# Kernel optimization log

Measured on AMD Instinct MI355X. Metric: run time of the kernel, lower is better.

## Reference

```python
import jax, jax.numpy as jnp
import numpy as np

TEMPERATURE = 0.07
MARGIN = 0.2
EPS = 1e-8  # matches torch F.cosine_similarity eps


def _cosine_matrix(a, b):
    # a: (N, D), b: (M, D) -> (N, M) pairwise cosine similarity
    an = a / jnp.clip(jnp.linalg.norm(a, axis=-1, keepdims=True), EPS)
    bn = b / jnp.clip(jnp.linalg.norm(b, axis=-1, keepdims=True), EPS)
    return an @ bn.T


def setup_inputs() -> dict:
    key = jax.random.key(0)
    k1, k2, k3 = jax.random.split(key, 3)
    return {
        "step_embeddings": jax.random.normal(k1, (8192, 1024), dtype=jnp.float32),
        "modal_embeddings": jax.random.normal(k2, (4096, 1024), dtype=jnp.float32),
        "negative_modal_embeddings": jax.random.normal(k3, (4096, 1024), dtype=jnp.float32),
    }


def reference(step_embeddings, modal_embeddings, negative_modal_embeddings):
    # --- step-modal alignment (max cosine sim per step, averaged) ---
    S = _cosine_matrix(step_embeddings, modal_embeddings)        # (N, M)
    per_step = S.max(axis=1)                                      # (N,)
    alignment = per_step.mean()

    # --- attention-weighted alignment (use_attention=True) ---
    logits = (step_embeddings @ modal_embeddings.T) / TEMPERATURE  # (N, M)
    attention = jax.nn.softmax(logits, axis=1)
    weighted_alignment = (S * attention).sum(axis=1).mean()

    # --- contrastive coherence against negatives ---
    Sn = _cosine_matrix(step_embeddings, negative_modal_embeddings)
    negative_alignment = Sn.max(axis=1).mean()
    positive_alignment = alignment
    contrastive_score = positive_alignment - negative_alignment
    margin_score = jax.nn.relu(contrastive_score - MARGIN)

    # --- per-step coherence (same max-cosine per step) ---
    min_step_coherence = per_step.min()

    # overall uses weighted_alignment (attention on), mixed with contrastive
    overall = 0.7 * weighted_alignment + 0.3 * contrastive_score

    return (alignment, weighted_alignment, attention, contrastive_score,
            margin_score, positive_alignment, negative_alignment,
            per_step, min_step_coherence, overall)
```

## Files before the change

### kernel.cpp

```cpp
#include <hip/hip_runtime.h>
#include <cmath>


#define WAVE 64

typedef __bf16 bf16x8_t __attribute__((ext_vector_type(8)));
typedef __bf16 bf16x4_t __attribute__((ext_vector_type(4)));
typedef float f32x4_t __attribute__((ext_vector_type(4)));

__device__ __forceinline__ float wave_reduce_sum(float v) {
#pragma unroll
    for (int o = 32; o > 0; o >>= 1) v += __shfl_down(v, o, WAVE);
    return v;
}
__device__ __forceinline__ float wave_reduce_max(float v) {
#pragma unroll
    for (int o = 32; o > 0; o >>= 1) v = fmaxf(v, __shfl_down(v, o, WAVE));
    return v;
}
__device__ __forceinline__ float wave_reduce_min(float v) {
#pragma unroll
    for (int o = 32; o > 0; o >>= 1) v = fminf(v, __shfl_down(v, o, WAVE));
    return v;
}

__device__ __forceinline__ unsigned enc_f(float f) {
    unsigned u = __float_as_uint(f);
    return (u & 0x80000000u) ? ~u : (u | 0x80000000u);
}
__device__ __forceinline__ float dec_f(unsigned e) {
    unsigned u = (e & 0x80000000u) ? (e & 0x7fffffffu) : ~e;
    return __uint_as_float(u);
}

__global__ __launch_bounds__(256)
void convert_norms_kernel(const float* __restrict__ step,
                          const float* __restrict__ modal,
                          const float* __restrict__ negs,
                          char* __restrict__ arena,
                          float* __restrict__ ina, float* __restrict__ inb,
                          float* __restrict__ inn,
                          unsigned* __restrict__ negmax_u, int N, int M) {
    const int tid = threadIdx.x, lane = tid & 63, wv = tid >> 6;
    const int b = blockIdx.x * 4 + wv;
    const float* src;
    if (b < N)          src = step  + (size_t)b * 1024;
    else if (b < N + M) src = modal + (size_t)(b - N) * 1024;
    else                src = negs  + (size_t)(b - N - M) * 1024;

    char* cb = arena + (((size_t)(b >> 2)) << 14) + ((size_t)(b & 3) << 11) + 8192;
    float s = 0.0f;
#pragma unroll
    for (int q = 0; q < 4; q++) {
        const int idx = lane + q * 64;
        const float4 v = ((const float4*)src)[idx];
        bf16x4_t o;
        o[0] = (__bf16)v.x; o[1] = (__bf16)v.y;
        o[2] = (__bf16)v.z; o[3] = (__bf16)v.w;
        *(bf16x4_t*)(cb + (size_t)idx * 8) = o;
        s += v.x * v.x + v.y * v.y + v.z * v.z + v.w * v.w;
    }
    s = wave_reduce_sum(s);
    if (lane == 0) {
        const float inv = 1.0f / fmaxf(sqrtf(s), 1e-8f);
        if (b < N)          { ina[b] = inv; negmax_u[b] = 0u; }
        else if (b < N + M) inb[b - N] = inv;
        else                inn[b - N - M] = inv;
    }
}

#define GLD16(g, l)                                                       \
    __builtin_amdgcn_global_load_lds(                                     \
        (const __attribute__((address_space(1))) void*)(g),               \
        (__attribute__((address_space(3))) void*)(l), 16, 0, 0)

#define PIPE_BARRIER() asm volatile(                                      \
    "s_waitcnt vmcnt(0) lgkmcnt(0)\n\ts_barrier" ::: "memory")

__global__ __launch_bounds__(256, 2)
void gemm_fused_kernel(char* __restrict__ arena, int N, int M,
                       const float* __restrict__ inv_nn,
                       unsigned* __restrict__ negmax_u) {
    __shared__ __bf16 As[2][128 * 64];
    __shared__ __bf16 Bs[2][128 * 64];

    const int lin = blockIdx.x;
    const int nbn = (2 * M) >> 7;
    const int SBM = 32, SBN = 8, PER = SBM * SBN;
    const int sid = lin / PER;
    const int q   = lin % PER;
    const int bmi = q % SBM;
    const int bni = q / SBM;
    const int stn_per = nbn / SBN;
    const int bmg = sid / stn_per;
    const int stn = sid % stn_per;
    const int bm = (bmg * SBM + bmi) << 7;
    const int bn = (stn * SBN + bni) << 7;

    const int t = threadIdx.x, w = t >> 6, lane = t & 63;
    const int lane16 = lane & 15, lq = lane >> 4;
    const int wm = (w & 1) * 64, wn = (w >> 1) * 64;

    const int s_is_b  = w >> 1;
    const int rowbase = (w & 1) * 64;
    const int ln3 = lane >> 3;
    const int q_g = (lane & 7) ^ ln3;
    const int cbase = (s_is_b ? (N + bn) : bm) + rowbase;
    const int cc = cbase + ln3;
    const size_t off0 = (((size_t)(cc >> 2)) << 14) +
                        ((size_t)(cc & 3) << 11) + 8192 + (size_t)q_g * 16;
    const char* gbase = arena + off0;
    const int ldsoff = rowbase * 64;
    __bf16* ldsw0 = (s_is_b ? Bs[0] : As[0]) + ldsoff;
    __bf16* ldsw1 = (s_is_b ? Bs[1] : As[1]) + ldsoff;

    f32x4_t acc[4][4];
#pragma unroll
    for (int i = 0; i < 4; i++)
#pragma unroll
        for (int j = 0; j < 4; j++) acc[i][j] = (f32x4_t){0.f, 0.f, 0.f, 0.f};

    const int sxr = lane16 & 7;

#pragma unroll
    for (int r = 0; r < 8; r++)
        GLD16(gbase + (size_t)r * 32768, ldsw0 + r * 512);

    for (int it = 0; it < 16; ++it) {
        PIPE_BARRIER();
        const int cur = it & 1;

        if (it + 1 < 16) {
            const size_t k0b = (size_t)(it + 1) * 128;
            __bf16* ldsw = cur ? ldsw0 : ldsw1;
#pragma unroll
            for (int r = 0; r < 8; r++)
                GLD16(gbase + (size_t)r * 32768 + k0b, ldsw + r * 512);
        }

        bf16x8_t af[2][4], bf[2][4];
#pragma unroll
        for (int kk = 0; kk < 2; kk++) {
            const int qo = ((lq + kk * 4) ^ sxr) * 8;
#pragma unroll
            for (int i = 0; i < 4; i++)
                af[kk][i] = *(const bf16x8_t*)&As[cur][(wm + i * 16 + lane16) * 64 + qo];
#pragma unroll
            for (int j = 0; j < 4; j++)
                bf[kk][j] = *(const bf16x8_t*)&Bs[cur][(wn + j * 16 + lane16) * 64 + qo];
        }

#pragma unroll
        for (int kk = 0; kk < 2; kk++)
#pragma unroll
            for (int i = 0; i < 4; i++)
#pragma unroll
                for (int j = 0; j < 4; j++)
                    acc[i][j] = __builtin_amdgcn_mfma_f32_16x16x32_bf16(
                        af[kk][i], bf[kk][j], acc[i][j], 0, 0, 0);
    }

    if (bn < M) {
#pragma unroll
        for (int i = 0; i < 4; i++) {
#pragma unroll
            for (int r = 0; r < 4; r++) {
                const int grow = bm + wm + i * 16 + lq * 4 + r;
                __bf16* dst = (__bf16*)(arena + ((size_t)grow << 14)) +
                              bn + wn + lane16;
#pragma unroll
                for (int j = 0; j < 4; j++)
                    dst[j * 16] = (__bf16)acc[i][j][r];
            }
        }
    } else {
        float invn[4];
#pragma unroll
        for (int j = 0; j < 4; j++)
            invn[j] = inv_nn[(bn - M) + wn + j * 16 + lane16];
#pragma unroll
        for (int i = 0; i < 4; i++) {
#pragma unroll
            for (int r = 0; r < 4; r++) {
                float v = acc[i][0][r] * invn[0];
                v = fmaxf(v, acc[i][1][r] * invn[1]);
                v = fmaxf(v, acc[i][2][r] * invn[2]);
                v = fmaxf(v, acc[i][3][r] * invn[3]);
#pragma unroll
                for (int o = 8; o > 0; o >>= 1)
                    v = fmaxf(v, __shfl_xor(v, o, WAVE));
                if (lane16 == 0)
                    atomicMax(&negmax_u[bm + wm + i * 16 + lq * 4 + r], enc_f(v));
            }
        }
    }
}

#define CUT 2.0f
#define MAXCAND 64

__global__ __launch_bounds__(256)
void softmax_fix_kernel(char* __restrict__ arena, const float* __restrict__ step,
                        const float* __restrict__ modal,
                        const float* __restrict__ ina, const float* __restrict__ inb,
                        float* __restrict__ perstep, float* __restrict__ wout,
                        float* __restrict__ attn) {
    const int row = blockIdx.x, tid = threadIdx.x;
    const int lane = tid & 63, wv = tid >> 6;

    __shared__ float srow_s[1024];
    __shared__ float red[8];
    __shared__ float bcast[2];
    __shared__ int   cand[MAXCAND];
    __shared__ float exact[MAXCAND];
    __shared__ int   cnt;

    if (tid == 0) cnt = 0;
    ((float4*)srow_s)[tid] = ((const float4*)(step + (size_t)row * 1024))[tid];

    const __bf16* gb = (const __bf16*)(arena + ((size_t)row << 14));
    float vals[16];
    float invn[16];
#pragma unroll
    for (int g = 0; g < 4; g++) {
        const bf16x4_t v = *(const bf16x4_t*)(gb + g * 1024 + tid * 4);
        const float4 x = *(const float4*)(inb + g * 1024 + tid * 4);
        vals[g * 4 + 0] = (float)v[0]; vals[g * 4 + 1] = (float)v[1];
        vals[g * 4 + 2] = (float)v[2]; vals[g * 4 + 3] = (float)v[3];
        invn[g * 4 + 0] = x.x; invn[g * 4 + 1] = x.y;
        invn[g * 4 + 2] = x.z; invn[g * 4 + 3] = x.w;
    }

    float dmax = -3.4e38f;
#pragma unroll
    for (int j = 0; j < 16; j++) dmax = fmaxf(dmax, vals[j]);
    float wm = wave_reduce_max(dmax);
    if (lane == 0) red[wv] = wm;
    __syncthreads();
    if (tid == 0) bcast[0] = fmaxf(fmaxf(red[0], red[1]), fmaxf(red[2], red[3]));
    __syncthreads();
    const float m0 = bcast[0];

    const float thr = m0 - CUT;
#pragma unroll
    for (int g = 0; g < 4; g++)
#pragma unroll
        for (int u = 0; u < 4; u++) {
            if (vals[g * 4 + u] >= thr) {
                const int pos = atomicAdd(&cnt, 1);
                if (pos < MAXCAND) cand[pos] = g * 1024 + tid * 4 + u;
            }
        }
    __syncthreads();
    const int nc = min(cnt, MAXCAND);

    for (int i = wv; i < nc; i += 4) {
        const float* mrow = modal + (size_t)cand[i] * 1024;
        float p = 0.0f;
#pragma unroll
        for (int q = 0; q < 16; q++) {
            const int idx = lane + q * 64;
            p = fmaf(srow_s[idx], mrow[idx], p);
        }
        p = wave_reduce_sum(p);
        if (lane == 0) exact[i] = p;
    }
    __syncthreads();

    for (int i = 0; i < nc; i++) {
        const int c = cand[i];
        if (((c & 1023) >> 2) == tid) vals[(c >> 10) * 4 + (c & 3)] = exact[i];
    }

    float dmax2 = -3.4e38f, cmax = -3.4e38f;
#pragma unroll
    for (int j = 0; j < 16; j++) {
        dmax2 = fmaxf(dmax2, vals[j]);
        cmax = fmaxf(cmax, vals[j] * invn[j]);
    }
    float wg = wave_reduce_max(dmax2);
    float wc = wave_reduce_max(cmax);
    if (lane == 0) { red[wv] = wg; red[4 + wv] = wc; }
    __syncthreads();
    if (tid == 0) {
        bcast[0] = fmaxf(fmaxf(red[0], red[1]), fmaxf(red[2], red[3]));
        bcast[1] = fmaxf(fmaxf(red[4], red[5]), fmaxf(red[6], red[7]));
    }
    __syncthreads();
    const float invT = 1.0f / 0.07f;
    const float mlog = bcast[0] * invT;
    const float cmaxAll = bcast[1];

    float evals[16];
    float lsum = 0.0f;
#pragma unroll
    for (int j = 0; j < 16; j++) {
        const float e = __expf(vals[j] * invT - mlog);
        evals[j] = e;
        lsum += e;
    }
    lsum = wave_reduce_sum(lsum);
    __syncthreads();
    if (lane == 0) red[wv] = lsum;
    __syncthreads();
    if (tid == 0) bcast[0] = red[0] + red[1] + red[2] + red[3];
    __syncthreads();
    const float invZ = 1.0f / bcast[0];

    float* arow = attn + (size_t)row * 4096;
    float wacc = 0.0f;
#pragma unroll
    for (int g = 0; g < 4; g++) {
        float4 o;
        const float a0 = evals[g * 4 + 0] * invZ, a1 = evals[g * 4 + 1] * invZ;
        const float a2 = evals[g * 4 + 2] * invZ, a3 = evals[g * 4 + 3] * invZ;
        o.x = a0; o.y = a1; o.z = a2; o.w = a3;
        *(float4*)(arow + g * 1024 + tid * 4) = o;
        wacc += a0 * vals[g * 4 + 0] * invn[g * 4 + 0];
        wacc += a1 * vals[g * 4 + 1] * invn[g * 4 + 1];
        wacc += a2 * vals[g * 4 + 2] * invn[g * 4 + 2];
        wacc += a3 * vals[g * 4 + 3] * invn[g * 4 + 3];
    }
    wacc = wave_reduce_sum(wacc);
    __syncthreads();
    if (lane == 0) red[wv] = wacc;
    __syncthreads();
    if (tid == 0) {
        const float inv_na = ina[row];
        perstep[row] = cmaxAll * inv_na;
        wout[row] = (red[0] + red[1] + red[2] + red[3]) * inv_na;
    }
}

__global__ __launch_bounds__(1024)
void finalize_kernel(const float* __restrict__ perstep, const float* __restrict__ w,
                     const unsigned* __restrict__ negmax_u,
                     const float* __restrict__ ina, float* __restrict__ out,
                     int N, size_t NM) {
    float s_a = 0.0f, s_w = 0.0f, s_n = 0.0f, mn = 3.4e38f;
    for (int i = threadIdx.x; i < N; i += 1024) {
        const float p = perstep[i];
        s_a += p;
        s_w += w[i];
        s_n += dec_f(negmax_u[i]) * ina[i];
        mn = fminf(mn, p);
    }
    s_a = wave_reduce_sum(s_a);
    s_w = wave_reduce_sum(s_w);
    s_n = wave_reduce_sum(s_n);
    mn  = wave_reduce_min(mn);
    __shared__ float ra[16], rw[16], rn[16], rm[16];
    const int lane = threadIdx.x & 63, wv = threadIdx.x >> 6;
    if (lane == 0) { ra[wv] = s_a; rw[wv] = s_w; rn[wv] = s_n; rm[wv] = mn; }
    __syncthreads();
    if (threadIdx.x == 0) {
        float ta = 0, tw = 0, tn = 0, tm = 3.4e38f;
#pragma unroll
        for (int i = 0; i < 16; i++) {
            ta += ra[i]; tw += rw[i]; tn += rn[i]; tm = fminf(tm, rm[i]);
        }
        const float inv = 1.0f / (float)N;
        const float alignment = ta * inv;
        const float weighted  = tw * inv;
        const float neg       = tn * inv;
        const float contrast  = alignment - neg;
        const float margin    = fmaxf(contrast - 0.2f, 0.0f);
        const float overall   = 0.7f * weighted + 0.3f * contrast;
        out[0] = alignment;
        out[1] = weighted;
        float* p = out + 2 + NM;
        p[0] = contrast;
        p[1] = margin;
        p[2] = alignment;
        p[3] = neg;
        p[4 + N] = tm;
        p[5 + N] = overall;
    }
}

extern "C" void kernel_launch(void* const* d_in, const int* in_sizes, int n_in,
                              void* d_out, int out_size, void* d_ws, size_t ws_size,
                              hipStream_t stream) {
    const float* step  = (const float*)d_in[0];
    const float* modal = (const float*)d_in[1];
    const float* negs  = (const float*)d_in[2];
    float* out = (float*)d_out;

    const int K = 1024;
    const int N = in_sizes[0] / K;
    const int M = in_sizes[1] / K;
    const size_t NM = (size_t)N * (size_t)M;

    float* ina        = (float*)d_ws;
    float* inb        = ina + N;
    float* inn        = inb + M;
    unsigned* negmax  = (unsigned*)(inn + M);
    float* wsum       = (float*)(negmax + N);

    char* arena    = (char*)d_out + 16;
    float* attn    = out + 2;
    float* perstep = out + 2 + NM + 4;

    convert_norms_kernel<<<(N + 2 * M) / 4, 256, 0, stream>>>(
        step, modal, negs, arena, ina, inb, inn, negmax, N, M);

    const int nblocks = (N / 128) * ((2 * M) / 128);
    gemm_fused_kernel<<<nblocks, 256, 0, stream>>>(arena, N, M, inn, negmax);

    softmax_fix_kernel<<<N, 256, 0, stream>>>(arena, step, modal, ina, inb,
                                              perstep, wsum, attn);

    finalize_kernel<<<1, 1024, 0, stream>>>(perstep, wsum, negmax, ina, out, N, NM);
}
```

Baseline: 381.0 us.

## Enlarge GEMM tile to 256x256 with 8-wave ping-pong MFMA/load interleaving

```diff
diff --git a/kernel.cpp b/kernel.cpp
--- a/kernel.cpp
+++ b/kernel.cpp
@@ -74,100 +74,152 @@
         (const __attribute__((address_space(1))) void*)(g),               \
         (__attribute__((address_space(3))) void*)(l), 16, 0, 0)
 
-#define PIPE_BARRIER() asm volatile(                                      \
-    "s_waitcnt vmcnt(0) lgkmcnt(0)\n\ts_barrier" ::: "memory")
-
-__global__ __launch_bounds__(256, 2)
+#define BAR()   asm volatile("s_barrier" ::: "memory")
+#define LGKM0() asm volatile("s_waitcnt lgkmcnt(0)" ::: "memory")
+#define VMW(n)  asm volatile("s_waitcnt vmcnt(" #n ")" ::: "memory")
+
+#define STAGE_A(Ab, kt)                                                   \
+    _Pragma("unroll")                                                     \
+    for (int h = 0; h < 2; h++)                                           \
+    _Pragma("unroll")                                                     \
+      for (int c = 0; c < 2; c++)                                         \
+        GLD16(arena + srcA[h][c] + (size_t)(kt) * 128,                    \
+              (Ab) + h * 8192 + c * 4096 + w * 512);
+
+#define STAGE_B(Bb, kt)                                                   \
+    _Pragma("unroll")                                                     \
+    for (int h = 0; h < 2; h++)                                           \
+    _Pragma("unroll")                                                     \
+      for (int c = 0; c < 2; c++)                                         \
+        GLD16(arena + srcB[h][c] + (size_t)(kt) * 128,                    \
+              (Bb) + h * 8192 + c * 4096 + w * 512);
+
+#define READ_A(g, Ab)                                                     \
+    _Pragma("unroll")                                                     \
+    for (int ii = 0; ii < 4; ii++)                                        \
+    _Pragma("unroll")                                                     \
+      for (int kk = 0; kk < 2; kk++)                                      \
+        af[ii][kk] = *(const bf16x8_t*)&(Ab)[arow0 + (g) * 4096 +         \
+                                             ii * 1024 + koff[kk]];
+
+#define READ_B(j0, dst, Bb)                                               \
+    _Pragma("unroll")                                                     \
+    for (int jj = 0; jj < 2; jj++)                                        \
+    _Pragma("unroll")                                                     \
+      for (int kk = 0; kk < 2; kk++)                                      \
+        dst[jj][kk] = *(const bf16x8_t*)&(Bb)[brow0 + ((j0) + jj) * 1024 +\
+                                              koff[kk]];
+
+#define MFMA_Q(i0, j0, bsrc)                                              \
+    __builtin_amdgcn_s_setprio(1);                                        \
+    _Pragma("unroll")                                                     \
+    for (int kk = 0; kk < 2; kk++)                                        \
+    _Pragma("unroll")                                                     \
+      for (int ii = 0; ii < 4; ii++)                                      \
+      _Pragma("unroll")                                                   \
+        for (int jj = 0; jj < 2; jj++)                                    \
+          acc[(i0) + ii][(j0) + jj] =                                     \
+              __builtin_amdgcn_mfma_f32_16x16x32_bf16(                    \
+                  af[ii][kk], bsrc[jj][kk], acc[(i0) + ii][(j0) + jj],    \
+                  0, 0, 0);                                               \
+    __builtin_amdgcn_s_setprio(0);
+
+#define TILE(Ab, Bb, ktpre, pre)                                          \
+                                                             \
+    READ_A(0, Ab);                                                        \
+    READ_B(0, bf01, Bb);                                                  \
+    BAR(); LGKM0();                                                       \
+    MFMA_Q(0, 0, bf01);                                                   \
+    BAR();                                                                \
+                                                             \
+    READ_B(2, bf23, Bb);                                                  \
+    BAR(); LGKM0();                                                       \
+    MFMA_Q(0, 2, bf23);                                                   \
+    BAR();                                                                \
+     \
+    READ_A(1, Ab);                                                        \
+    if (pre) { STAGE_B(Bb, ktpre); }                                      \
+    BAR(); LGKM0();                                                       \
+    MFMA_Q(4, 0, bf01);                                                   \
+    BAR();                                                                \
+     \
+    if (pre) { STAGE_A(Ab, ktpre); }                                      \
+    BAR();                                                                \
+    MFMA_Q(4, 2, bf23);                                                   \
+    if (pre) { VMW(8); } else { VMW(0); }                                 \
+    BAR();
+
+__global__ __launch_bounds__(512, 2)
 void gemm_fused_kernel(char* __restrict__ arena, int N, int M,
                        const float* __restrict__ inv_nn,
                        unsigned* __restrict__ negmax_u) {
-    __shared__ __bf16 As[2][128 * 64];
-    __shared__ __bf16 Bs[2][128 * 64];
+    __shared__ __bf16 As[2][256 * 64];
+    __shared__ __bf16 Bs[2][256 * 64];
 
     const int lin = blockIdx.x;
-    const int nbn = (2 * M) >> 7;
-    const int SBM = 32, SBN = 8, PER = SBM * SBN;
-    const int sid = lin / PER;
-    const int q   = lin % PER;
-    const int bmi = q % SBM;
-    const int bni = q / SBM;
-    const int stn_per = nbn / SBN;
-    const int bmg = sid / stn_per;
-    const int stn = sid % stn_per;
-    const int bm = (bmg * SBM + bmi) << 7;
-    const int bn = (stn * SBN + bni) << 7;
+    const int sid = lin >> 5, qq = lin & 31;
+    const int bmi = qq & 7, bni = qq >> 3;
+    const int bmg = sid >> 3, stn = sid & 7;
+    const int bm = (bmg * 8 + bmi) << 8;
+    const int bn = (stn * 4 + bni) << 8;
 
     const int t = threadIdx.x, w = t >> 6, lane = t & 63;
     const int lane16 = lane & 15, lq = lane >> 4;
-    const int wm = (w & 1) * 64, wn = (w >> 1) * 64;
-
-    const int s_is_b  = w >> 1;
-    const int rowbase = (w & 1) * 64;
-    const int ln3 = lane >> 3;
-    const int q_g = (lane & 7) ^ ln3;
-    const int cbase = (s_is_b ? (N + bn) : bm) + rowbase;
-    const int cc = cbase + ln3;
-    const size_t off0 = (((size_t)(cc >> 2)) << 14) +
-                        ((size_t)(cc & 3) << 11) + 8192 + (size_t)q_g * 16;
-    const char* gbase = arena + off0;
-    const int ldsoff = rowbase * 64;
-    __bf16* ldsw0 = (s_is_b ? Bs[0] : As[0]) + ldsoff;
-    __bf16* ldsw1 = (s_is_b ? Bs[1] : As[1]) + ldsoff;
-
-    f32x4_t acc[4][4];
-#pragma unroll
-    for (int i = 0; i < 4; i++)
-#pragma unroll
-        for (int j = 0; j < 4; j++) acc[i][j] = (f32x4_t){0.f, 0.f, 0.f, 0.f};
+    const int wm = w >> 2, wn = w & 3;
+
+    const int l3 = lane >> 3, ol = lane & 7;
+    const int og = ol ^ l3;
+    unsigned srcA[2][2], srcB[2][2];
+#pragma unroll
+    for (int h = 0; h < 2; h++)
+#pragma unroll
+      for (int c = 0; c < 2; c++) {
+        const int ga = bm + h * 128 + c * 64 + w * 8 + l3;
+        srcA[h][c] = ((unsigned)(ga >> 2) << 14) + ((unsigned)(ga & 3) << 11)
+                     + 8192u + (unsigned)og * 16u;
+        const int gb = N + bn + h * 128 + c * 64 + w * 8 + l3;
+        srcB[h][c] = ((unsigned)(gb >> 2) << 14) + ((unsigned)(gb & 3) << 11)
+                     + 8192u + (unsigned)og * 16u;
+      }
 
     const int sxr = lane16 & 7;
-
-#pragma unroll
-    for (int r = 0; r < 8; r++)
-        GLD16(gbase + (size_t)r * 32768, ldsw0 + r * 512);
-
-    for (int it = 0; it < 16; ++it) {
-        PIPE_BARRIER();
-        const int cur = it & 1;
-
-        if (it + 1 < 16) {
-            const size_t k0b = (size_t)(it + 1) * 128;
-            __bf16* ldsw = cur ? ldsw0 : ldsw1;
-#pragma unroll
-            for (int r = 0; r < 8; r++)
-                GLD16(gbase + (size_t)r * 32768 + k0b, ldsw + r * 512);
-        }
-
-        bf16x8_t af[2][4], bf[2][4];
-#pragma unroll
-        for (int kk = 0; kk < 2; kk++) {
-            const int qo = ((lq + kk * 4) ^ sxr) * 8;
-#pragma unroll
-            for (int i = 0; i < 4; i++)
-                af[kk][i] = *(const bf16x8_t*)&As[cur][(wm + i * 16 + lane16) * 64 + qo];
-#pragma unroll
-            for (int j = 0; j < 4; j++)
-                bf[kk][j] = *(const bf16x8_t*)&Bs[cur][(wn + j * 16 + lane16) * 64 + qo];
-        }
-
-#pragma unroll
-        for (int kk = 0; kk < 2; kk++)
-#pragma unroll
-            for (int i = 0; i < 4; i++)
-#pragma unroll
-                for (int j = 0; j < 4; j++)
-                    acc[i][j] = __builtin_amdgcn_mfma_f32_16x16x32_bf16(
-                        af[kk][i], bf[kk][j], acc[i][j], 0, 0, 0);
+    int koff[2];
+#pragma unroll
+    for (int kk = 0; kk < 2; kk++) koff[kk] = ((lq + 4 * kk) ^ sxr) * 8;
+    const int arow0 = wm * 8192 + lane16 * 64;
+    const int brow0 = wn * 4096 + lane16 * 64;
+
+    f32x4_t acc[8][4];
+#pragma unroll
+    for (int i = 0; i < 8; i++)
+#pragma unroll
+      for (int j = 0; j < 4; j++) acc[i][j] = (f32x4_t){0.f, 0.f, 0.f, 0.f};
+
+    bf16x8_t af[4][2], bf01[2][2], bf23[2][2];
+
+    __bf16* const A0 = As[0]; __bf16* const A1 = As[1];
+    __bf16* const B0 = Bs[0]; __bf16* const B1 = Bs[1];
+
+    STAGE_A(A0, 0); STAGE_B(B0, 0);
+    STAGE_A(A1, 1); STAGE_B(B1, 1);
+    VMW(8);
+    BAR();
+
+    for (int it = 0; it < 8; ++it) {
+        const int pre = (it < 7);
+        const int k2 = 2 * it + 2, k3 = 2 * it + 3;
+        TILE(A0, B0, k2, pre)
+        TILE(A1, B1, k3, pre)
     }
 
     if (bn < M) {
 #pragma unroll
-        for (int i = 0; i < 4; i++) {
+        for (int i = 0; i < 8; i++) {
 #pragma unroll
             for (int r = 0; r < 4; r++) {
-                const int grow = bm + wm + i * 16 + lq * 4 + r;
+                const int grow = bm + wm * 128 + i * 16 + lq * 4 + r;
                 __bf16* dst = (__bf16*)(arena + ((size_t)grow << 14)) +
-                              bn + wn + lane16;
+                              bn + wn * 64 + lane16;
 #pragma unroll
                 for (int j = 0; j < 4; j++)
                     dst[j * 16] = (__bf16)acc[i][j][r];
@@ -177,9 +229,9 @@
         float invn[4];
 #pragma unroll
         for (int j = 0; j < 4; j++)
-            invn[j] = inv_nn[(bn - M) + wn + j * 16 + lane16];
-#pragma unroll
-        for (int i = 0; i < 4; i++) {
+            invn[j] = inv_nn[(bn - M) + wn * 64 + j * 16 + lane16];
+#pragma unroll
+        for (int i = 0; i < 8; i++) {
 #pragma unroll
             for (int r = 0; r < 4; r++) {
                 float v = acc[i][0][r] * invn[0];
@@ -190,7 +242,8 @@
                 for (int o = 8; o > 0; o >>= 1)
                     v = fmaxf(v, __shfl_xor(v, o, WAVE));
                 if (lane16 == 0)
-                    atomicMax(&negmax_u[bm + wm + i * 16 + lq * 4 + r], enc_f(v));
+                    atomicMax(&negmax_u[bm + wm * 128 + i * 16 + lq * 4 + r],
+                              enc_f(v));
             }
         }
     }
@@ -404,8 +457,8 @@
     convert_norms_kernel<<<(N + 2 * M) / 4, 256, 0, stream>>>(
         step, modal, negs, arena, ina, inb, inn, negmax, N, M);
 
-    const int nblocks = (N / 128) * ((2 * M) / 128);
-    gemm_fused_kernel<<<nblocks, 256, 0, stream>>>(arena, N, M, inn, negmax);
+    const int nblocks = (N >> 8) * ((2 * M) >> 8);
+    gemm_fused_kernel<<<nblocks, 512, 0, stream>>>(arena, N, M, inn, negmax);
 
     softmax_fix_kernel<<<N, 256, 0, stream>>>(arena, step, modal, ina, inb,
                                               perstep, wsum, attn);
```

Result: no change. 380.9 us (-0.0%).
